# Performance work log

Hardware: AMD Instinct MI355X
Metric: run time of the kernel (lower is better)

## Reference

```python
import jax, jax.numpy as jnp
import numpy as np

EMBED, HEADS, LEVELS, POINTS, MLP = 256, 8, 3, 4, 4
SHAPES = [(60, 80), (30, 40), (15, 20)]  # (H, W) per level


def layer_norm(x, g, b):
    m = jnp.mean(x, -1, keepdims=True)
    v = jnp.mean((x - m) ** 2, -1, keepdims=True)
    return (x - m) * jax.lax.rsqrt(v + 1e-5) * g + b


def _bilinear(v, H, W, gx, gy):
    # v: [B,h,H*W,dh]; gx,gy: [B,h,Nq,P] absolute pixel coords (grid_sample align_corners=False, zero padding)
    x0 = jnp.floor(gx); y0 = jnp.floor(gy)
    wx = gx - x0; wy = gy - y0

    def g(xi, yi):
        valid = ((xi >= 0) & (xi < W) & (yi >= 0) & (yi < H)).astype(v.dtype)
        idx = jnp.clip(yi, 0, H - 1) * W + jnp.clip(xi, 0, W - 1)
        B, h, Nq, P = idx.shape
        out = jnp.take_along_axis(v, idx.reshape(B, h, Nq * P)[..., None], axis=2)
        return out.reshape(B, h, Nq, P, -1) * valid[..., None]

    x0i = x0.astype(jnp.int32); y0i = y0.astype(jnp.int32)
    return (g(x0i, y0i) * ((1 - wx) * (1 - wy))[..., None]
            + g(x0i + 1, y0i) * (wx * (1 - wy))[..., None]
            + g(x0i, y0i + 1) * ((1 - wx) * wy)[..., None]
            + g(x0i + 1, y0i + 1) * (wx * wy)[..., None])


def setup_inputs() -> dict:
    key = jax.random.key(0)
    ks = jax.random.split(key, 16)
    B, Nq, C = 2, 8192, EMBED
    Nv = sum(h * w for h, w in SHAPES)
    s = 0.02
    d = {
        'query': jax.random.normal(ks[0], (B, Nq, C), jnp.float32),
        'value': jax.random.normal(ks[1], (B, Nv, C), jnp.float32),
        'query_pos': jax.random.normal(ks[2], (B, Nq, C), jnp.float32),
        'ref_pts': jax.random.uniform(ks[3], (B, Nq, LEVELS, 2), jnp.float32),
        'spatial_shapes': jnp.array(SHAPES, jnp.int32),
        'level_start_index': jnp.array(np.cumsum([0] + [h * w for h, w in SHAPES[:-1]]), jnp.int32),
        'g1': jnp.ones((C,), jnp.float32), 'b1': jnp.zeros((C,), jnp.float32),
        'Wo': s * jax.random.normal(ks[4], (C, HEADS * LEVELS * POINTS * 2), jnp.float32),
        'bo': jnp.zeros((HEADS * LEVELS * POINTS * 2,), jnp.float32),
        'Wa': s * jax.random.normal(ks[5], (C, HEADS * LEVELS * POINTS), jnp.float32),
        'ba': jnp.zeros((HEADS * LEVELS * POINTS,), jnp.float32),
        'Wv': s * jax.random.normal(ks[6], (C, C), jnp.float32), 'bv': jnp.zeros((C,), jnp.float32),
        'Wp': s * jax.random.normal(ks[7], (C, C), jnp.float32), 'bp': jnp.zeros((C,), jnp.float32),
        'g2': jnp.ones((C,), jnp.float32), 'b2': jnp.zeros((C,), jnp.float32),
        'Wf1': s * jax.random.normal(ks[8], (C, MLP * C), jnp.float32), 'bf1': jnp.zeros((MLP * C,), jnp.float32),
        'Wf2': s * jax.random.normal(ks[9], (MLP * C, C), jnp.float32), 'bf2': jnp.zeros((C,), jnp.float32),
    }
    return d


def reference(query, value, query_pos, ref_pts, spatial_shapes, level_start_index,
              g1, b1, Wo, bo, Wa, ba, Wv, bv, Wp, bp, g2, b2, Wf1, bf1, Wf2, bf2):
    B, Nq, C = query.shape
    dh = C // HEADS
    shapes = np.asarray(spatial_shapes).tolist()
    starts = np.asarray(level_start_index).tolist()

    qn = layer_norm(query, g1, b1)           # pre-norm
    qa = qn + query_pos                       # positional embedding inside attn
    offs = (qa @ Wo + bo).reshape(B, Nq, HEADS, LEVELS, POINTS, 2)
    aw = jax.nn.softmax((qa @ Wa + ba).reshape(B, Nq, HEADS, LEVELS * POINTS), -1)
    aw = aw.reshape(B, Nq, HEADS, LEVELS, POINTS)
    v = (value @ Wv + bv).reshape(B, -1, HEADS, dh).transpose(0, 2, 1, 3)  # [B,h,Nv,dh]

    # offset_normalizer = (W, H) per level
    norm = jnp.array([[w, h] for h, w in shapes], jnp.float32)
    loc = ref_pts[:, :, None, :, None, :] + offs / norm[None, None, None, :, None, :]

    out = jnp.zeros((B, Nq, HEADS, dh), query.dtype)
    for l, (H, W) in enumerate(shapes):
        vl = jax.lax.dynamic_slice_in_dim(v, starts[l], H * W, axis=2)
        gl = loc[:, :, :, l].transpose(0, 2, 1, 3, 4)   # [B,h,Nq,P,2]
        gx = gl[..., 0] * W - 0.5
        gy = gl[..., 1] * H - 0.5
        sampled = _bilinear(vl, H, W, gx, gy)            # [B,h,Nq,P,dh]
        out = out + jnp.einsum('bhqpd,bqhp->bqhd', sampled, aw[:, :, :, l])

    attn = out.reshape(B, Nq, C) @ Wp + bp + qn          # output proj + mmcv internal residual (identity=norm1(query))
    q = query + attn                                     # layer residual
    q2 = layer_norm(q, g2, b2)
    return q + (jax.nn.gelu(q2 @ Wf1 + bf1, approximate=False) @ Wf2 + bf2)
```

## Files before the change

### kernel.cpp

```cpp
#include <hip/hip_runtime.h>
#include <math.h>


typedef short short8 __attribute__((ext_vector_type(8)));
typedef short s16x4 __attribute__((ext_vector_type(4)));
typedef __bf16 bf16x8 __attribute__((ext_vector_type(8)));
typedef float f32x4 __attribute__((ext_vector_type(4)));

__device__ __forceinline__ short f2b(float f) {
  unsigned u = __builtin_bit_cast(unsigned, f);
  u += 0x7fffu + ((u >> 16) & 1u);
  return (short)(u >> 16);
}
__device__ __forceinline__ float b2f(short s) {
  unsigned u = ((unsigned)(unsigned short)s) << 16;
  return __builtin_bit_cast(float, u);
}
__device__ __forceinline__ void b8f(short8 s, float* f) {
  const uint4 u = __builtin_bit_cast(uint4, s);
  f[0] = __builtin_bit_cast(float, u.x << 16);
  f[1] = __builtin_bit_cast(float, u.x & 0xffff0000u);
  f[2] = __builtin_bit_cast(float, u.y << 16);
  f[3] = __builtin_bit_cast(float, u.y & 0xffff0000u);
  f[4] = __builtin_bit_cast(float, u.z << 16);
  f[5] = __builtin_bit_cast(float, u.z & 0xffff0000u);
  f[6] = __builtin_bit_cast(float, u.w << 16);
  f[7] = __builtin_bit_cast(float, u.w & 0xffff0000u);
}

__device__ __forceinline__ f32x4 mfma16(short8 a, short8 b, f32x4 c) {
  return __builtin_amdgcn_mfma_f32_16x16x32_bf16(
      __builtin_bit_cast(bf16x8, a), __builtin_bit_cast(bf16x8, b), c, 0, 0, 0);
}

typedef __attribute__((address_space(3))) unsigned int lds_u32;
typedef const __attribute__((address_space(1))) unsigned int glb_u32;
__device__ __forceinline__ void glds16(const void* g, void* l) {
  __builtin_amdgcn_global_load_lds((glb_u32*)g, (lds_u32*)l, 16, 0, 0);
}

__device__ __forceinline__ float gelu1(float v) {
  return 0.5f * v * (1.f + erff(v * 0.70710678118654752f));
}

template <int EPI>
__device__ __forceinline__ void gemm64_core(
    int bx, int by,
    const short* __restrict__ A, const short* __restrict__ Bt,
    const float* __restrict__ bias, const float* __restrict__ bias2,
    const void* __restrict__ add1,
    void* __restrict__ Cout, int M, int Nreal, int ldc, int K, char* smem)
{
  short* sA = (short*)smem;
  short* sB = sA + 4096;
  float* sf = (float*)smem;

  const int t = threadIdx.x;
  const int wave = t >> 6, lane = t & 63;
  const int quad = lane >> 4, l16 = lane & 15;
  const int wm = (wave & 1) * 32, wn = (wave >> 1) * 64;
  const int m0 = by * 64, n0 = bx * 128;

  f32x4 acc[2][4];
#pragma unroll
  for (int i = 0; i < 2; i++)
#pragma unroll
    for (int j = 0; j < 4; j++) acc[i][j] = (f32x4){0.f, 0.f, 0.f, 0.f};

  const int srow = lane >> 3, pos = lane & 7;
  const int chunk = (pos + srow) & 7;
  const short* gA = A + (size_t)(m0 + wave * 16 + srow) * K + chunk * 8;
  const short* gB = Bt + (size_t)(n0 + wave * 32 + srow) * K + chunk * 8;

  const int nk = K >> 6;
  for (int kt = 0; kt < nk; ++kt) {
    if (kt) __syncthreads();
    const int ko = kt * 64;
#pragma unroll
    for (int g = 0; g < 2; ++g)
      glds16(gA + ko + (size_t)(g * 8) * K, sA + (wave * 16 + g * 8) * 64);
#pragma unroll
    for (int g = 0; g < 4; ++g)
      glds16(gB + ko + (size_t)(g * 8) * K, sB + (wave * 32 + g * 8) * 64);
    __syncthreads();
#pragma unroll
    for (int kk = 0; kk < 2; ++kk) {
      short8 af[2], bf[4];
      const int c = kk * 4 + quad;
#pragma unroll
      for (int i = 0; i < 2; i++) {
        const int lrA = wm + i * 16 + l16;
        af[i] = *(const short8*)&sA[lrA * 64 + ((c - lrA) & 7) * 8];
      }
#pragma unroll
      for (int j = 0; j < 4; j++) {
        const int lrB = wn + j * 16 + l16;
        bf[j] = *(const short8*)&sB[lrB * 64 + ((c - lrB) & 7) * 8];
      }
#pragma unroll
      for (int i = 0; i < 2; i++)
#pragma unroll
        for (int j = 0; j < 4; j++) acc[i][j] = mfma16(bf[j], af[i], acc[i][j]);
    }
  }
  __syncthreads();

#pragma unroll
  for (int b = 0; b < 2; ++b) {
    if (wm == b * 32) {
#pragma unroll
      for (int i = 0; i < 2; ++i) {
        const int rr = i * 16 + l16;
#pragma unroll
        for (int j = 0; j < 4; ++j)
          *(f32x4*)&sf[rr * 132 + wn + quad * 4 + j * 16] = acc[i][j];
      }
    }
    __syncthreads();
#pragma unroll
    for (int r2 = 0; r2 < 4; ++r2) {
      const int fidx = r2 * 1024 + t * 4;
      const int row = fidx >> 7, col = fidx & 127;
      const int gm = m0 + b * 32 + row;
      const int cc = n0 + col;
      if (gm < M && cc < Nreal) {
        const float4 v = *(const float4*)&sf[row * 132 + col];
        float4 bb;
        if (EPI == 4) bb = (cc < 192) ? *(const float4*)(bias + cc)
                                      : *(const float4*)(bias2 + cc - 192);
        else bb = *(const float4*)(bias + cc);
        float v0 = v.x + bb.x, v1 = v.y + bb.y, v2 = v.z + bb.z, v3 = v.w + bb.w;
        if (EPI == 1) {
          v0 = gelu1(v0); v1 = gelu1(v1); v2 = gelu1(v2); v3 = gelu1(v3);
          s16x4 o; o.x = f2b(v0); o.y = f2b(v1); o.z = f2b(v2); o.w = f2b(v3);
          *(s16x4*)((short*)Cout + (size_t)gm * ldc + cc) = o;
        } else if (EPI == 5 || EPI == 4) {
          s16x4 o; o.x = f2b(v0); o.y = f2b(v1); o.z = f2b(v2); o.w = f2b(v3);
          *(s16x4*)((short*)Cout + (size_t)gm * ldc + cc) = o;
        } else {
          if (EPI == 3) {
            const float4 a1 = *(const float4*)((const float*)add1 + (size_t)gm * ldc + cc);
            v0 += a1.x; v1 += a1.y; v2 += a1.z; v3 += a1.w;
          }
          *(float4*)((float*)Cout + (size_t)gm * ldc + cc) =
              make_float4(v0, v1, v2, v3);
        }
      }
    }
    __syncthreads();
  }
}

template <int EPI>
__global__ __launch_bounds__(256) void gemm64_k(
    const short* __restrict__ A, const short* __restrict__ Bt,
    const float* __restrict__ bias, const void* __restrict__ add1,
    void* __restrict__ Cout, int M, int Nreal, int ldc, int K)
{
  __shared__ __align__(16) char smem[24576];
  gemm64_core<EPI>(blockIdx.x, blockIdx.y, A, Bt, bias, nullptr, add1,
                   Cout, M, Nreal, ldc, K, smem);
}

__global__ __launch_bounds__(256) void gemm_oa_v(
    const short* __restrict__ qa, const short* __restrict__ wt_oa,
    const float* __restrict__ bo, const float* __restrict__ ba,
    short* __restrict__ oabuf,
    const short* __restrict__ valbf, const short* __restrict__ wt_v,
    const float* __restrict__ bv, short* __restrict__ vproj)
{
  __shared__ __align__(16) char smem[24576];
  const int idx = blockIdx.x;
  if (idx < 768) {
    gemm64_core<4>(idx % 3, idx / 3, qa, wt_oa, bo, ba, nullptr,
                   oabuf, 16384, 288, 288, 256, smem);
  } else {
    const int r = idx - 768;
    gemm64_core<5>(r % 2, r / 2, valbf, wt_v, bv, nullptr, nullptr,
                   vproj, 12600, 256, 256, 256, smem);
  }
}

__global__ __launch_bounds__(256) void gemm_wp_ln2(
    const short* __restrict__ A, const short* __restrict__ Bt,
    const float* __restrict__ bias,
    const short* __restrict__ qnb, const float* __restrict__ query,
    const float* __restrict__ g2, const float* __restrict__ b2v,
    float* __restrict__ qbuf, short* __restrict__ q2)
{
  __shared__ __align__(16) char smem[36864];
  short* sA = (short*)smem;
  short* sB = sA + 2048;
  float* sf = (float*)smem;

  const int t = threadIdx.x;
  const int wave = t >> 6, lane = t & 63;
  const int quad = lane >> 4, l16 = lane & 15;
  const int wm = (wave & 1) * 16, wn = (wave >> 1) * 128;
  const int m0 = blockIdx.x * 32;
  const int K = 256;

  f32x4 acc[8];
#pragma unroll
  for (int j = 0; j < 8; j++) acc[j] = (f32x4){0.f, 0.f, 0.f, 0.f};

  const int srow = lane >> 3, pos = lane & 7;
  const int chunk = (pos + srow) & 7;
  const short* gA = A + (size_t)(m0 + wave * 8 + srow) * K + chunk * 8;
  const short* gB = Bt + (size_t)(wave * 64 + srow) * K + chunk * 8;

  for (int kt = 0; kt < 4; ++kt) {
    if (kt) __syncthreads();
    const int ko = kt * 64;
    glds16(gA + ko, sA + (wave * 8) * 64);
#pragma unroll
    for (int g = 0; g < 8; ++g)
      glds16(gB + ko + (size_t)(g * 8) * K, sB + (wave * 64 + g * 8) * 64);
    __syncthreads();
#pragma unroll
    for (int kk = 0; kk < 2; ++kk) {
      const int c = kk * 4 + quad;
      const int lrA = wm + l16;
      const short8 af = *(const short8*)&sA[lrA * 64 + ((c - lrA) & 7) * 8];
      short8 bf[8];
#pragma unroll
      for (int j = 0; j < 8; j++) {
        const int lrB = wn + j * 16 + l16;
        bf[j] = *(const short8*)&sB[lrB * 64 + ((c - lrB) & 7) * 8];
      }
#pragma unroll
      for (int j = 0; j < 8; j++) acc[j] = mfma16(bf[j], af, acc[j]);
    }
  }
  __syncthreads();

#pragma unroll
  for (int j = 0; j < 8; j++)
    *(f32x4*)&sf[(wm + l16) * 260 + wn + j * 16 + quad * 4] = acc[j];
  __syncthreads();

  const float4 bb   = *(const float4*)(bias + lane * 4);
  const float4 gv   = *(const float4*)(g2 + lane * 4);
  const float4 b2f4 = *(const float4*)(b2v + lane * 4);
#pragma unroll
  for (int rr = 0; rr < 8; ++rr) {
    const int row = wave * 8 + rr;
    const int gm = m0 + row;
    const float4 a = *(const float4*)&sf[row * 260 + lane * 4];
    const s16x4 qn = *(const s16x4*)(qnb + (size_t)gm * 256 + lane * 4);
    const float4 qv = *(const float4*)(query + (size_t)gm * 256 + lane * 4);
    float q0 = a.x + bb.x + b2f(qn.x) + qv.x;
    float q1 = a.y + bb.y + b2f(qn.y) + qv.y;
    float q2f = a.z + bb.z + b2f(qn.z) + qv.z;
    float q3 = a.w + bb.w + b2f(qn.w) + qv.w;
    float s = q0 + q1 + q2f + q3;
#pragma unroll
    for (int o = 32; o; o >>= 1) s += __shfl_xor(s, o);
    const float mean = s * (1.f / 256.f);
    const float d0 = q0 - mean, d1 = q1 - mean, d2 = q2f - mean, d3 = q3 - mean;
    float ss = d0 * d0 + d1 * d1 + d2 * d2 + d3 * d3;
#pragma unroll
    for (int o = 32; o; o >>= 1) ss += __shfl_xor(ss, o);
    const float inv = rsqrtf(ss * (1.f / 256.f) + 1e-5f);
    *(float4*)(qbuf + (size_t)gm * 256 + lane * 4) = make_float4(q0, q1, q2f, q3);
    s16x4 o2;
    o2.x = f2b(d0 * inv * gv.x + b2f4.x);
    o2.y = f2b(d1 * inv * gv.y + b2f4.y);
    o2.z = f2b(d2 * inv * gv.z + b2f4.z);
    o2.w = f2b(d3 * inv * gv.w + b2f4.w);
    *(s16x4*)(q2 + (size_t)gm * 256 + lane * 4) = o2;
  }
}

__global__ __launch_bounds__(256) void prep_all(
    const float* __restrict__ Wo, const float* __restrict__ Wa,
    const float* __restrict__ Wv, const float* __restrict__ Wp,
    const float* __restrict__ Wf1, const float* __restrict__ Wf2,
    short* __restrict__ t_oa, short* __restrict__ t_v, short* __restrict__ t_p,
    short* __restrict__ t_f1, short* __restrict__ t_f2,
    const float* __restrict__ value, short* __restrict__ valbf,
    const float* __restrict__ query, const float* __restrict__ query_pos,
    const float* __restrict__ g1, const float* __restrict__ b1,
    short* __restrict__ qnb, short* __restrict__ qa)
{
  __shared__ float tile[32][33];
  const int t = threadIdx.x;
  const int blk = blockIdx.x;

  if (blk < 1792) {
    const int bxa = blk & 255, bya = blk >> 8;
    int K, N, noff; const float* src; short* dst;
    switch (bya) {
      case 0: src = Wo;      dst = t_oa; K = 256;  N = 192;  noff = 0;   break;
      case 1: src = Wa;      dst = t_oa; K = 256;  N = 96;   noff = 192; break;
      case 2: src = nullptr; dst = t_oa; K = 256;  N = 96;   noff = 288; break;
      case 3: src = Wv;      dst = t_v;  K = 256;  N = 256;  noff = 0;   break;
      case 4: src = Wp;      dst = t_p;  K = 256;  N = 256;  noff = 0;   break;
      case 5: src = Wf1;     dst = t_f1; K = 256;  N = 1024; noff = 0;   break;
      default: src = Wf2;    dst = t_f2; K = 1024; N = 256;  noff = 0;   break;
    }
    const int tilesK = K >> 5;
    const int nt = tilesK * (N >> 5);
    if (bxa >= nt) return;
    const int tk = bxa % tilesK, tn = bxa / tilesK;
    const int k0 = tk * 32, n0 = tn * 32;
    const int r = t >> 3, c4 = (t & 7) * 4;
    float4 v = make_float4(0.f, 0.f, 0.f, 0.f);
    if (src) v = *(const float4*)(src + (size_t)(k0 + r) * N + n0 + c4);
    tile[r][c4] = v.x; tile[r][c4 + 1] = v.y; tile[r][c4 + 2] = v.z; tile[r][c4 + 3] = v.w;
    __syncthreads();
    const int nn = t >> 3, kc = (t & 7) * 4;
    s16x4 o;
    o.x = f2b(tile[kc][nn]); o.y = f2b(tile[kc + 1][nn]);
    o.z = f2b(tile[kc + 2][nn]); o.w = f2b(tile[kc + 3][nn]);
    *(s16x4*)(dst + (size_t)(noff + n0 + nn) * K + k0 + kc) = o;
  } else if (blk < 1792 + 3169) {
    const int i = ((blk - 1792) * 256 + t) * 4;
    if (i >= 12672 * 256) return;
    s16x4 o = (s16x4){0, 0, 0, 0};
    if (i < 12600 * 256) {
      float4 v = *(const float4*)(value + i);
      o.x = f2b(v.x); o.y = f2b(v.y); o.z = f2b(v.z); o.w = f2b(v.w);
    }
    *(s16x4*)(valbf + i) = o;
  } else {
    const int row  = (blk - 4961) * 4 + (t >> 6);
    const int lane = t & 63;
    const float4 v = ((const float4*)(query + (size_t)row * 256))[lane];
    float s = v.x + v.y + v.z + v.w;
#pragma unroll
    for (int o = 32; o; o >>= 1) s += __shfl_xor(s, o);
    const float mean = s * (1.f / 256.f);
    const float dx = v.x - mean, dy = v.y - mean, dz = v.z - mean, dw = v.w - mean;
    float s2 = dx * dx + dy * dy + dz * dz + dw * dw;
#pragma unroll
    for (int o = 32; o; o >>= 1) s2 += __shfl_xor(s2, o);
    const float inv = rsqrtf(s2 * (1.f / 256.f) + 1e-5f);
    const float4 gv = ((const float4*)g1)[lane];
    const float4 bv = ((const float4*)b1)[lane];
    const float4 o1 = make_float4(dx * inv * gv.x + bv.x, dy * inv * gv.y + bv.y,
                                  dz * inv * gv.z + bv.z, dw * inv * gv.w + bv.w);
    s16x4 ob; ob.x = f2b(o1.x); ob.y = f2b(o1.y); ob.z = f2b(o1.z); ob.w = f2b(o1.w);
    ((s16x4*)(qnb + (size_t)row * 256))[lane] = ob;
    const float4 pv = ((const float4*)(query_pos + (size_t)row * 256))[lane];
    s16x4 op;
    op.x = f2b(o1.x + pv.x); op.y = f2b(o1.y + pv.y);
    op.z = f2b(o1.z + pv.z); op.w = f2b(o1.w + pv.w);
    ((s16x4*)(qa + (size_t)row * 256))[lane] = op;
  }
}

__global__ __launch_bounds__(256) void deform_fused(
    const short* __restrict__ vproj, const short* __restrict__ oa,
    const float* __restrict__ refp, short* __restrict__ out)
{
  __shared__ int4 sIdx[768];
  __shared__ s16x4 sW[768];
  const int t = threadIdx.x;

  if (t < 64) {
    const int row = blockIdx.x * 8 + (t >> 3), h = t & 7;
    const short* oarow = oa + (size_t)row * 288;
    float off[24];
    {
      const short8* op = (const short8*)(oarow + h * 24);
      b8f(op[0], off); b8f(op[1], off + 8); b8f(op[2], off + 16);
    }
    float lg[12];
    {
      const s16x4* ap = (const s16x4*)(oarow + 192 + h * 12);
#pragma unroll
      for (int i = 0; i < 3; i++) {
        const s16x4 v = ap[i];
        lg[i * 4] = b2f(v.x); lg[i * 4 + 1] = b2f(v.y);
        lg[i * 4 + 2] = b2f(v.z); lg[i * 4 + 3] = b2f(v.w);
      }
    }
    const float* rp = refp + (size_t)row * 6;
    const float Rx[3] = {rp[0], rp[2], rp[4]}, Ry[3] = {rp[1], rp[3], rp[5]};
    float mx = lg[0];
#pragma unroll
    for (int i = 1; i < 12; i++) mx = fmaxf(mx, lg[i]);
    float sum = 0.f;
#pragma unroll
    for (int i = 0; i < 12; i++) { lg[i] = __expf(lg[i] - mx); sum += lg[i]; }
    const float inv = 1.f / sum;
    const int b = row >> 13;
    const int Hs[3] = {60, 30, 15}, Ws[3] = {80, 40, 20}, St[3] = {0, 4800, 6000};
#pragma unroll
    for (int p = 0; p < 12; p++) {
      const int l = p >> 2;
      const int W = Ws[l], H = Hs[l];
      const float gx = Rx[l] * W + off[p * 2]     - 0.5f;
      const float gy = Ry[l] * H + off[p * 2 + 1] - 0.5f;
      const float x0f = floorf(gx), y0f = floorf(gy);
      const float wx = gx - x0f, wy = gy - y0f;
      const int x0 = (int)x0f, y0 = (int)y0f;
      const float aw = lg[p] * inv;
      float cw[4] = {(1.f - wx) * (1.f - wy), wx * (1.f - wy),
                     (1.f - wx) * wy, wx * wy};
      const int base = b * 6300 + St[l];
      int ci[4];
#pragma unroll
      for (int k = 0; k < 4; k++) {
        const int xx = x0 + (k & 1), yy = y0 + (k >> 1);
        const bool valid = (xx >= 0) & (xx < W) & (yy >= 0) & (yy < H);
        const int xc = min(max(xx, 0), W - 1);
        const int yc = min(max(yy, 0), H - 1);
        ci[k] = ((base + yc * W + xc) << 8) + h * 32;
        cw[k] = valid ? cw[k] * aw : 0.f;
      }
      sIdx[t * 12 + p] = make_int4(ci[0], ci[1], ci[2], ci[3]);
      s16x4 wv; wv.x = f2b(cw[0]); wv.y = f2b(cw[1]); wv.z = f2b(cw[2]); wv.w = f2b(cw[3]);
      sW[t * 12 + p] = wv;
    }
  }
  __syncthreads();

  const int lu = t >> 2, c4 = (t & 3) * 8;
  float acc[8];
#pragma unroll
  for (int i = 0; i < 8; i++) acc[i] = 0.f;
#pragma unroll 2
  for (int p = 0; p < 12; p++) {
    const int4 idx = sIdx[lu * 12 + p];
    const s16x4 wb = sW[lu * 12 + p];
    const float w0 = b2f(wb.x), w1 = b2f(wb.y), w2 = b2f(wb.z), w3 = b2f(wb.w);
    const short8 v0 = *(const short8*)(vproj + idx.x + c4);
    const short8 v1 = *(const short8*)(vproj + idx.y + c4);
    const short8 v2 = *(const short8*)(vproj + idx.z + c4);
    const short8 v3 = *(const short8*)(vproj + idx.w + c4);
    float f0[8], f1[8], f2[8], f3[8];
    b8f(v0, f0); b8f(v1, f1); b8f(v2, f2); b8f(v3, f3);
#pragma unroll
    for (int j = 0; j < 8; j++)
      acc[j] += w0 * f0[j] + w1 * f1[j] + w2 * f2[j] + w3 * f3[j];
  }
  short8 o;
#pragma unroll
  for (int j = 0; j < 8; j++) o[j] = f2b(acc[j]);
  *(short8*)(out + (size_t)(blockIdx.x * 256 + t) * 8) = o;
}

extern "C" void kernel_launch(void* const* d_in, const int* in_sizes, int n_in,
                              void* d_out, int out_size, void* d_ws, size_t ws_size,
                              hipStream_t stream)
{
  const float* query     = (const float*)d_in[0];
  const float* value     = (const float*)d_in[1];
  const float* query_pos = (const float*)d_in[2];
  const float* ref_pts   = (const float*)d_in[3];
  const float* g1  = (const float*)d_in[6];
  const float* b1  = (const float*)d_in[7];
  const float* Wo  = (const float*)d_in[8];
  const float* bo  = (const float*)d_in[9];
  const float* Wa  = (const float*)d_in[10];
  const float* ba  = (const float*)d_in[11];
  const float* Wv  = (const float*)d_in[12];
  const float* bv  = (const float*)d_in[13];
  const float* Wp  = (const float*)d_in[14];
  const float* bp  = (const float*)d_in[15];
  const float* g2  = (const float*)d_in[16];
  const float* b2  = (const float*)d_in[17];
  const float* Wf1 = (const float*)d_in[18];
  const float* bf1 = (const float*)d_in[19];
  const float* Wf2 = (const float*)d_in[20];
  const float* bf2 = (const float*)d_in[21];

  char* ws = (char*)d_ws;
  short* wt_oa   = (short*)(ws + 0);
  short* wt_v    = (short*)(ws + 196608);
  short* wt_p    = (short*)(ws + 327680);
  short* wt_f1   = (short*)(ws + 458752);
  short* wt_f2   = (short*)(ws + 983040);
  short* qnb     = (short*)(ws + 1507328);
  short* qa      = (short*)(ws + 18284544);
  short* oabuf   = (short*)(ws + 26673152);
  short* vproj   = (short*)(ws + 45547520);
  short* sampled = (short*)(ws + 51998720);
  float* qbuf    = (float*)(ws + 60387328);
  short* valbf   = (short*)(ws + 77164544);
  short* q2      = qa;
  short* hidden  = (short*)(ws + 26673152);
  float* outp = (float*)d_out;

  prep_all<<<9057, 256, 0, stream>>>(Wo, Wa, Wv, Wp, Wf1, Wf2,
                                     wt_oa, wt_v, wt_p, wt_f1, wt_f2,
                                     value, valbf, query, query_pos,
                                     g1, b1, qnb, qa);
  gemm_oa_v<<<1162, 256, 0, stream>>>(qa, wt_oa, bo, ba, oabuf,
                                      valbf, wt_v, bv, vproj);
  deform_fused<<<2048, 256, 0, stream>>>(vproj, oabuf, ref_pts, sampled);
  gemm_wp_ln2<<<512, 256, 0, stream>>>(sampled, wt_p, bp, qnb, query,
                                       g2, b2, qbuf, q2);
  gemm64_k<1><<<dim3(8, 256), 256, 0, stream>>>(q2, wt_f1, bf1, nullptr,
                                                hidden, 16384, 1024, 1024, 256);
  gemm64_k<3><<<dim3(2, 256), 256, 0, stream>>>(hidden, wt_f2, bf2, qbuf,
                                                outp, 16384, 256, 256, 1024);
}
```

Baseline: 223.4 us.

## Fuse FFN GEMMs into one kernel keeping GELU hidden in LDS

```diff
diff --git a/kernel.cpp b/kernel.cpp
--- a/kernel.cpp
+++ b/kernel.cpp
@@ -130,36 +130,12 @@
                                       : *(const float4*)(bias2 + cc - 192);
         else bb = *(const float4*)(bias + cc);
         float v0 = v.x + bb.x, v1 = v.y + bb.y, v2 = v.z + bb.z, v3 = v.w + bb.w;
-        if (EPI == 1) {
-          v0 = gelu1(v0); v1 = gelu1(v1); v2 = gelu1(v2); v3 = gelu1(v3);
-          s16x4 o; o.x = f2b(v0); o.y = f2b(v1); o.z = f2b(v2); o.w = f2b(v3);
-          *(s16x4*)((short*)Cout + (size_t)gm * ldc + cc) = o;
-        } else if (EPI == 5 || EPI == 4) {
-          s16x4 o; o.x = f2b(v0); o.y = f2b(v1); o.z = f2b(v2); o.w = f2b(v3);
-          *(s16x4*)((short*)Cout + (size_t)gm * ldc + cc) = o;
-        } else {
-          if (EPI == 3) {
-            const float4 a1 = *(const float4*)((const float*)add1 + (size_t)gm * ldc + cc);
-            v0 += a1.x; v1 += a1.y; v2 += a1.z; v3 += a1.w;
-          }
-          *(float4*)((float*)Cout + (size_t)gm * ldc + cc) =
-              make_float4(v0, v1, v2, v3);
-        }
+        s16x4 o; o.x = f2b(v0); o.y = f2b(v1); o.z = f2b(v2); o.w = f2b(v3);
+        *(s16x4*)((short*)Cout + (size_t)gm * ldc + cc) = o;
       }
     }
     __syncthreads();
   }
-}
-
-template <int EPI>
-__global__ __launch_bounds__(256) void gemm64_k(
-    const short* __restrict__ A, const short* __restrict__ Bt,
-    const float* __restrict__ bias, const void* __restrict__ add1,
-    void* __restrict__ Cout, int M, int Nreal, int ldc, int K)
-{
-  __shared__ __align__(16) char smem[24576];
-  gemm64_core<EPI>(blockIdx.x, blockIdx.y, A, Bt, bias, nullptr, add1,
-                   Cout, M, Nreal, ldc, K, smem);
 }
 
 __global__ __launch_bounds__(256) void gemm_oa_v(
@@ -272,6 +248,134 @@
   }
 }
 
+__global__ __launch_bounds__(512, 2) void fused_mlp(
+    const short* __restrict__ q2,
+    const short* __restrict__ wf1,
+    const float* __restrict__ b1v,
+    const short* __restrict__ wf2,
+    const float* __restrict__ b2v,
+    const float* __restrict__ qbuf,
+    float* __restrict__ outp)
+{
+  __shared__ __align__(16) char smem[147456];
+  short* H  = (short*)smem;
+  short* sA = (short*)(smem + 131072);
+  float* sf = (float*)smem;
+
+  const int t = threadIdx.x;
+  const int w = t >> 6, lane = t & 63;
+  const int quad = lane >> 4, l16 = lane & 15;
+  const int m0 = blockIdx.x * 64;
+
+  for (int p = 0; p < 2; ++p) {
+    f32x4 acc[4][4];
+#pragma unroll
+    for (int i = 0; i < 4; i++)
+#pragma unroll
+      for (int j = 0; j < 4; j++) acc[i][j] = (f32x4){0.f, 0.f, 0.f, 0.f};
+
+    for (int ap = 0; ap < 2; ++ap) {
+      __syncthreads();
+#pragma unroll
+      for (int g = 0; g < 2; ++g) {
+        const int row = w * 8 + g * 4 + (lane >> 4);
+        const int pp  = lane & 15;
+        const int cl  = (pp & ~7) | ((pp + row) & 7);
+        glds16(q2 + (size_t)(m0 + row) * 256 + (size_t)(ap * 16 + cl) * 8,
+               sA + w * 1024 + g * 512 + lane * 8);
+      }
+      __syncthreads();
+#pragma unroll
+      for (int kk = 0; kk < 4; ++kk) {
+        const int cl = kk * 4 + quad;
+        const int cg = ap * 16 + cl;
+        short8 bfr[4], afr[4];
+#pragma unroll
+        for (int j = 0; j < 4; ++j) {
+          const int n1 = w * 8 + p * 4 + j;
+          bfr[j] = *(const short8*)(wf1 + ((size_t)n1 * 32 + cg) * 128 + l16 * 8);
+        }
+#pragma unroll
+        for (int i = 0; i < 4; ++i) {
+          const int r = i * 16 + l16;
+          const int pos = (cl & ~7) | ((cl - r) & 7);
+          afr[i] = *(const short8*)(sA + r * 128 + pos * 8);
+        }
+#pragma unroll
+        for (int i = 0; i < 4; ++i)
+#pragma unroll
+          for (int j = 0; j < 4; ++j) acc[i][j] = mfma16(bfr[j], afr[i], acc[i][j]);
+      }
+    }
+#pragma unroll
+    for (int j = 0; j < 4; ++j) {
+      const int colb = w * 128 + p * 64 + j * 16 + quad * 4;
+      const float4 bb = *(const float4*)(b1v + colb);
+      const int c = colb >> 3;
+#pragma unroll
+      for (int i = 0; i < 4; ++i) {
+        const int r = i * 16 + l16;
+        const int pos = (c & ~7) | ((c - r) & 7);
+        s16x4 o;
+        o.x = f2b(gelu1(acc[i][j].x + bb.x));
+        o.y = f2b(gelu1(acc[i][j].y + bb.y));
+        o.z = f2b(gelu1(acc[i][j].z + bb.z));
+        o.w = f2b(gelu1(acc[i][j].w + bb.w));
+        *(s16x4*)(H + r * 1024 + pos * 8 + (colb & 7)) = o;
+      }
+    }
+  }
+  __syncthreads();
+
+  f32x4 acc2[4][2];
+#pragma unroll
+  for (int i = 0; i < 4; i++)
+#pragma unroll
+    for (int j = 0; j < 2; j++) acc2[i][j] = (f32x4){0.f, 0.f, 0.f, 0.f};
+
+#pragma unroll 4
+  for (int kk = 0; kk < 32; ++kk) {
+    const int c = kk * 4 + quad;
+    short8 bfr[2], afr[4];
+#pragma unroll
+    for (int j = 0; j < 2; ++j) {
+      const int n1 = w * 2 + j;
+      bfr[j] = *(const short8*)(wf2 + ((size_t)n1 * 128 + c) * 128 + l16 * 8);
+    }
+#pragma unroll
+    for (int i = 0; i < 4; ++i) {
+      const int r = i * 16 + l16;
+      const int pos = (c & ~7) | ((c - r) & 7);
+      afr[i] = *(const short8*)(H + r * 1024 + pos * 8);
+    }
+#pragma unroll
+    for (int i = 0; i < 4; ++i)
+#pragma unroll
+      for (int j = 0; j < 2; ++j) acc2[i][j] = mfma16(bfr[j], afr[i], acc2[i][j]);
+  }
+  __syncthreads();
+
+#pragma unroll
+  for (int i = 0; i < 4; ++i)
+#pragma unroll
+    for (int j = 0; j < 2; ++j)
+      *(f32x4*)&sf[(i * 16 + l16) * 260 + w * 32 + j * 16 + quad * 4] = acc2[i][j];
+  __syncthreads();
+
+#pragma unroll
+  for (int rep = 0; rep < 8; ++rep) {
+    const int fidx = rep * 2048 + t * 4;
+    const int row = fidx >> 8, col = fidx & 255;
+    const int gm = m0 + row;
+    const float4 v  = *(const float4*)&sf[row * 260 + col];
+    const float4 bb = *(const float4*)(b2v + col);
+    const float4 qv = *(const float4*)(qbuf + (size_t)gm * 256 + col);
+    *(float4*)(outp + (size_t)gm * 256 + col) =
+        make_float4(v.x + bb.x + qv.x, v.y + bb.y + qv.y,
+                    v.z + bb.z + qv.z, v.w + bb.w + qv.w);
+  }
+}
+
 __global__ __launch_bounds__(256) void prep_all(
     const float* __restrict__ Wo, const float* __restrict__ Wa,
     const float* __restrict__ Wv, const float* __restrict__ Wp,
@@ -299,6 +403,7 @@
       case 5: src = Wf1;     dst = t_f1; K = 256;  N = 1024; noff = 0;   break;
       default: src = Wf2;    dst = t_f2; K = 1024; N = 256;  noff = 0;   break;
     }
+    const bool fragpack = (bya >= 5);
     const int tilesK = K >> 5;
     const int nt = tilesK * (N >> 5);
     if (bxa >= nt) return;
@@ -313,7 +418,13 @@
     s16x4 o;
     o.x = f2b(tile[kc][nn]); o.y = f2b(tile[kc + 1][nn]);
     o.z = f2b(tile[kc + 2][nn]); o.w = f2b(tile[kc + 3][nn]);
-    *(s16x4*)(dst + (size_t)(noff + n0 + nn) * K + k0 + kc) = o;
+    if (fragpack) {
+      const int n = n0 + nn, k = k0 + kc;
+      *(s16x4*)(dst + ((size_t)(n >> 4) * (K >> 3) + (k >> 3)) * 128 +
+                (n & 15) * 8 + (k & 7)) = o;
+    } else {
+      *(s16x4*)(dst + (size_t)(noff + n0 + nn) * K + k0 + kc) = o;
+    }
   } else if (blk < 1792 + 3169) {
     const int i = ((blk - 1792) * 256 + t) * 4;
     if (i >= 12672 * 256) return;
@@ -481,7 +592,6 @@
   float* qbuf    = (float*)(ws + 60387328);
   short* valbf   = (short*)(ws + 77164544);
   short* q2      = qa;
-  short* hidden  = (short*)(ws + 26673152);
   float* outp = (float*)d_out;
 
   prep_all<<<9057, 256, 0, stream>>>(Wo, Wa, Wv, Wp, Wf1, Wf2,
@@ -493,8 +603,5 @@
   deform_fused<<<2048, 256, 0, stream>>>(vproj, oabuf, ref_pts, sampled);
   gemm_wp_ln2<<<512, 256, 0, stream>>>(sampled, wt_p, bp, qnb, query,
                                        g2, b2, qbuf, q2);
-  gemm64_k<1><<<dim3(8, 256), 256, 0, stream>>>(q2, wt_f1, bf1, nullptr,
-                                                hidden, 16384, 1024, 1024, 256);
-  gemm64_k<3><<<dim3(2, 256), 256, 0, stream>>>(hidden, wt_f2, bf2, qbuf,
-                                                outp, 16384, 256, 256, 1024);
-}
+  fused_mlp<<<256, 512, 0, stream>>>(q2, wt_f1, bf1, wt_f2, bf2, qbuf, outp);
+}
```

Measured after the change: 214.8 us. 3.9% less time.
